# Optimization experiments

Hardware: AMD Instinct MI355X
Metric: run time of the kernel (lower is better)

The kernel has to match this reference:

```python
import jax, jax.numpy as jnp
import numpy as np

B, S, D, H = 2, 2048, 1024, 16
HD = D // H
EPS = 1e-5


def setup_inputs() -> dict:
    key = jax.random.key(0)
    ks = jax.random.split(key, 12)
    s = 1.0 / np.sqrt(D)
    inp = {
        "q": jax.random.normal(ks[0], (B, S, D), jnp.float32),
        "k": jax.random.normal(ks[1], (B, S, D), jnp.float32),
        "v": jax.random.normal(ks[2], (B, S, D), jnp.float32),
        "mask": jnp.ones((B, S, S), jnp.int32),
        "Wq": jax.random.normal(ks[3], (D, D), jnp.float32) * s,
        "bq": jnp.zeros((D,), jnp.float32),
        "Wk": jax.random.normal(ks[4], (D, D), jnp.float32) * s,
        "bk": jnp.zeros((D,), jnp.float32),
        "Wv": jax.random.normal(ks[5], (D, D), jnp.float32) * s,
        "bv": jnp.zeros((D,), jnp.float32),
        "Wo": jax.random.normal(ks[6], (D, D), jnp.float32) * s,
        "bo": jnp.zeros((D,), jnp.float32),
        "gamma": jnp.ones((D,), jnp.float32),
        "beta": jnp.zeros((D,), jnp.float32),
    }
    return inp


def reference(q, k, v, mask, Wq, bq, Wk, bk, Wv, bv, Wo, bo, gamma, beta):
    residual = q
    # projections (torch Linear: x @ W.T + b)
    qh = (q @ Wq.T + bq).reshape(B, S, H, HD).transpose(0, 2, 1, 3)  # b h s d
    kh = (k @ Wk.T + bk).reshape(B, S, H, HD).transpose(0, 2, 1, 3)
    vh = (v @ Wv.T + bv).reshape(B, S, H, HD).transpose(0, 2, 1, 3)
    scores = jnp.einsum('bhid,bhjd->bhij', qh, kh) / jnp.sqrt(jnp.float32(HD))
    scores = jnp.where(mask[:, None, :, :] == 0, jnp.float32(-1e9), scores)
    attention = jax.nn.softmax(scores, axis=-1)  # dropout=0 (eval)
    context = jnp.einsum('bhij,bhjd->bhid', attention, vh)
    context = context.transpose(0, 2, 1, 3).reshape(B, S, D)
    out = context @ Wo.T + bo
    x = out + residual
    mu = jnp.mean(x, axis=-1, keepdims=True)
    var = jnp.mean(jnp.square(x - mu), axis=-1, keepdims=True)
    output = (x - mu) * jax.lax.rsqrt(var + EPS) * gamma + beta
    return (output, attention)
```

## Files before the change

kernel.cpp:

```cpp
#include <hip/hip_runtime.h>
#include <hip/hip_bf16.h>


typedef float f32x4 __attribute__((ext_vector_type(4)));
typedef short short8 __attribute__((ext_vector_type(8)));

#if __has_builtin(__builtin_amdgcn_exp2f)
#define EXP2(x) __builtin_amdgcn_exp2f(x)
#else
#define EXP2(x) exp2f(x)
#endif

#define QSCALE 0.18033688011112042f
#define MASKNEG -1.4426950408889634e9f

#define BAR_DRAIN16() asm volatile("s_waitcnt vmcnt(16) lgkmcnt(0)\ns_barrier" ::: "memory")
#define BAR_LGKM()    asm volatile("s_waitcnt lgkmcnt(0)\ns_barrier" ::: "memory")

__device__ __forceinline__ short f2bs(float f) {
  union { __hip_bfloat16 h; short s; } u;
  u.h = __float2bfloat16(f);
  return u.s;
}

__device__ __forceinline__ void async16(const void* g, void* l) {
  __builtin_amdgcn_global_load_lds(
      (const __attribute__((address_space(1))) unsigned int*)g,
      (__attribute__((address_space(3))) unsigned int*)l, 16, 0, 0);
}

__global__ __launch_bounds__(256) void cvt_mask_kernel(
    const float* __restrict__ q, const float* __restrict__ k, const float* __restrict__ v,
    const float* __restrict__ wq, const float* __restrict__ wk, const float* __restrict__ wv,
    const float* __restrict__ wo, short* __restrict__ dst,
    const int* __restrict__ mask, unsigned* __restrict__ bits, unsigned* __restrict__ flags) {
  if (blockIdx.x < 8192) {
    long base = (long)blockIdx.x * 2048;
    const float* src;
    if      (base <  4194304) src = q  + base;
    else if (base <  8388608) src = k  + (base - 4194304);
    else if (base < 12582912) src = v  + (base - 8388608);
    else if (base < 13631488) src = wq + (base - 12582912);
    else if (base < 14680064) src = wk + (base - 13631488);
    else if (base < 15728640) src = wv + (base - 14680064);
    else                      src = wo + (base - 15728640);
    int off = threadIdx.x * 8;
    float4 a = *(const float4*)(src + off);
    float4 b = *(const float4*)(src + off + 4);
    short8 o;
    o[0] = f2bs(a.x); o[1] = f2bs(a.y); o[2] = f2bs(a.z); o[3] = f2bs(a.w);
    o[4] = f2bs(b.x); o[5] = f2bs(b.y); o[6] = f2bs(b.z); o[7] = f2bs(b.w);
    *(short8*)(dst + base + off) = o;
  } else {
    int bid = blockIdx.x - 8192;
    int t = threadIdx.x, w = t >> 6, lane = t & 63;
    for (int it = 0; it < 16; ++it) {
      long gw = (long)it * 8192 + bid * 4 + w;
      long base = gw * 64;
      int mv = mask[base + lane];
      unsigned long long m = __ballot(mv != 0);
      if (lane == 0)  bits[gw * 2]     = (unsigned)m;
      if (lane == 32) bits[gw * 2 + 1] = (unsigned)(m >> 32);
      if (lane == 0 && m != 0xFFFFFFFFFFFFFFFFull) {
        long j = base & 2047, i = (base >> 11) & 2047, b = base >> 22;
        atomicOr(&flags[(int)(b * 256 + (i >> 7) * 16 + (j >> 7))], 1u);
      }
    }
  }
}

__global__ __launch_bounds__(256, 2) void proj_kernel(
    const short* __restrict__ Abase, const short* __restrict__ Wbase,
    const float* __restrict__ bq, const float* __restrict__ bk, const float* __restrict__ bv,
    short* __restrict__ Qh, short* __restrict__ Kh, short* __restrict__ Vt) {
  __shared__ __align__(16) short As[2][128 * 64];
  __shared__ __align__(16) short Bs[2][128 * 64];
  const int mode = blockIdx.z;
  const short* A = Abase + (size_t)mode * 4194304;
  const short* W = Wbase + (size_t)mode * 1048576;
  const float* bias = (mode == 0) ? bq : (mode == 1 ? bk : bv);
  const int t = threadIdx.x, w = t >> 6, lane = t & 63, g = lane >> 4, lc = lane & 15;
  const int wrow = (w >> 1) * 64, wcol = (w & 1) * 64;
  const int m0 = blockIdx.x * 128, n0 = blockIdx.y * 128;

#define PSTAGE(buf, k0)                                                                     \
  do {                                                                                      \
    _Pragma("unroll") for (int i_ = 0; i_ < 4; i_++) {                                      \
      int cb = i_ * 256 + w * 64, ch = cb + lane, row = ch >> 3, c = ch & 7;                \
      int so = ((c ^ (row & 7)) << 3);                                                      \
      async16(A + (size_t)(m0 + row) * 1024 + (k0) + so, (void*)&As[buf][cb << 3]);         \
      async16(W + (size_t)(n0 + row) * 1024 + (k0) + so, (void*)&Bs[buf][cb << 3]);         \
    }                                                                                       \
  } while (0)

  f32x4 acc[4][4] = {};
  PSTAGE(0, 0);
  __syncthreads();
  int pb = 0;
  for (int kt = 0; kt < 16; ++kt) {
    if (kt < 15) PSTAGE(pb ^ 1, (kt + 1) * 64);
#pragma unroll
    for (int kf = 0; kf < 2; ++kf) {
      short8 af[4], bf[4];
#pragma unroll
      for (int m = 0; m < 4; m++) {
        int row = wrow + m * 16 + lc;
        af[m] = *(const short8*)&As[pb][(row << 6) + (((kf * 4 + g) ^ (row & 7)) << 3)];
      }
#pragma unroll
      for (int n = 0; n < 4; n++) {
        int row = wcol + n * 16 + lc;
        bf[n] = *(const short8*)&Bs[pb][(row << 6) + (((kf * 4 + g) ^ (row & 7)) << 3)];
      }
      __builtin_amdgcn_s_setprio(1);
#pragma unroll
      for (int m = 0; m < 4; m++)
#pragma unroll
        for (int n = 0; n < 4; n++)
          acc[m][n] = __builtin_amdgcn_mfma_f32_16x16x32_bf16(af[m], bf[n], acc[m][n], 0, 0, 0);
      __builtin_amdgcn_s_setprio(0);
    }
    __syncthreads();
    pb ^= 1;
  }
#undef PSTAGE
#pragma unroll
  for (int n = 0; n < 4; n++) {
    const int col = n0 + wcol + n * 16 + lc;
    const float bv_ = bias[col];
    const int h = col >> 6, d = col & 63;
#pragma unroll
    for (int m = 0; m < 4; m++)
#pragma unroll
      for (int r = 0; r < 4; r++) {
        const int srow = m0 + wrow + m * 16 + g * 4 + r;
        const int b = srow >> 11, s = srow & 2047;
        float val = acc[m][n][r] + bv_;
        if (mode == 0)
          Qh[((size_t)(b * 16 + h) * 2048 + s) * 64 + d] = f2bs(val * QSCALE);
        else if (mode == 1)
          Kh[((size_t)(b * 16 + h) * 2048 + s) * 64 + d] = f2bs(val);
        else
          Vt[((size_t)(b * 16 + h) * 64 + d) * 2048 + s] = f2bs(val);
      }
  }
}

__global__ __launch_bounds__(256, 2) void attn_kernel(
    const short* __restrict__ Qh, const short* __restrict__ Kh, const short* __restrict__ Vt,
    const unsigned* __restrict__ mbits, const unsigned* __restrict__ mflags,
    float* __restrict__ Pout, short* __restrict__ ctx) {
  __shared__ __align__(16) short Ks[2][128 * 64];
  __shared__ __align__(16) short Vs[64 * 128];
  __shared__ __align__(16) short Ps[128 * 128];
  const int L = blockIdx.x;
  const int xcd = L & 7, idx = L >> 3;
  const int bh = xcd + ((idx >> 4) << 3);
  const int qb = idx & 15;
  const int b = bh >> 4, h = bh & 15;
  const int t = threadIdx.x, w = t >> 6, lane = t & 63, g = lane >> 4, lc = lane & 15;
  const short* Qp = Qh + (size_t)bh * 2048 * 64;
  const short* Kp = Kh + (size_t)bh * 2048 * 64;
  const short* Vp = Vt + (size_t)bh * 64 * 2048;
  float* Pb = Pout + ((size_t)bh * 2048 + qb * 128) * 2048;

  short8 qf[2][2];
#pragma unroll
  for (int qm = 0; qm < 2; qm++)
#pragma unroll
    for (int kf = 0; kf < 2; kf++)
      qf[qm][kf] = *(const short8*)(Qp + (size_t)(qb * 128 + w * 32 + qm * 16 + lc) * 64 + kf * 32 + g * 8);

#define STAGE_K(buf, j0)                                                                   \
  do {                                                                                     \
    _Pragma("unroll") for (int i_ = 0; i_ < 4; i_++) {                                     \
      int cb = i_ * 256 + w * 64, ch = cb + lane, row = ch >> 3, c = ch & 7;               \
      int sc = c ^ (row & 7) ^ ((row >> 3) & 7);                                           \
      async16(Kp + (size_t)((j0) + row) * 64 + (sc << 3), (void*)&Ks[buf][cb << 3]);       \
    }                                                                                      \
  } while (0)
#define STAGE_V(j0)                                                                        \
  do {                                                                                     \
    _Pragma("unroll") for (int i_ = 0; i_ < 4; i_++) {                                     \
      int cb = i_ * 256 + w * 64, ch = cb + lane, row = ch >> 4, c = ch & 15;              \
      async16(Vp + (size_t)row * 2048 + (j0) + ((c ^ (row & 15)) << 3), (void*)&Vs[cb << 3]); \
    }                                                                                      \
  } while (0)

  float lsum[2] = {0.f, 0.f};
  int kb = 0;
  STAGE_K(0, 0);
  __syncthreads();
  for (int it = 0; it < 16; ++it) {
    if (it < 15) STAGE_K(kb ^ 1, (it + 1) * 128);
    f32x4 acc[2][8] = {};
    __builtin_amdgcn_s_setprio(1);
#pragma unroll
    for (int kf = 0; kf < 2; kf++)
#pragma unroll
      for (int n = 0; n < 8; n++) {
        int row = n * 16 + lc;
        int sc = (kf * 4 + g) ^ (row & 7) ^ ((row >> 3) & 7);
        short8 kfr = *(const short8*)&Ks[kb][(row << 6) + (sc << 3)];
        acc[0][n] = __builtin_amdgcn_mfma_f32_16x16x32_bf16(kfr, qf[0][kf], acc[0][n], 0, 0, 0);
        acc[1][n] = __builtin_amdgcn_mfma_f32_16x16x32_bf16(kfr, qf[1][kf], acc[1][n], 0, 0, 0);
      }
    __builtin_amdgcn_s_setprio(0);
    unsigned flg = mflags[b * 256 + qb * 16 + it];
    if (flg) {
#pragma unroll
      for (int qm = 0; qm < 2; qm++) {
        int ig = qb * 128 + w * 32 + qm * 16 + lc;
        uint4 mw = *(const uint4*)(mbits + ((size_t)b * 2048 + ig) * 64 + it * 4);
#pragma unroll
        for (int n = 0; n < 8; n++) {
          unsigned bw = (n >> 1) == 0 ? mw.x : ((n >> 1) == 1 ? mw.y : ((n >> 1) == 2 ? mw.z : mw.w));
#pragma unroll
          for (int r = 0; r < 4; r++)
            if (!((bw >> (((n & 1) << 4) + g * 4 + r)) & 1u)) acc[qm][n][r] = MASKNEG;
        }
      }
    }
#pragma unroll
    for (int qm = 0; qm < 2; qm++) {
      float s_ = 0.f;
#pragma unroll
      for (int n = 0; n < 8; n++)
#pragma unroll
        for (int r = 0; r < 4; r++) s_ += EXP2(acc[qm][n][r]);
      s_ += __shfl_xor(s_, 16);
      s_ += __shfl_xor(s_, 32);
      lsum[qm] += s_;
    }
    __syncthreads();
    kb ^= 1;
  }
  float* ls = (float*)Vs;
  if (g == 0) { ls[w * 32 + lc] = lsum[0]; ls[w * 32 + 16 + lc] = lsum[1]; }
  __syncthreads();
  float linv[8];
#pragma unroll
  for (int qm = 0; qm < 2; qm++)
#pragma unroll
    for (int r = 0; r < 4; r++) linv[qm * 4 + r] = 1.0f / ls[w * 32 + qm * 16 + g * 4 + r];
  kb = 0;
  STAGE_K(0, 0);
  __syncthreads();

  f32x4 acco[2][4] = {};
  for (int it = 0; it < 16; ++it) {
    const int j0 = it * 128;
    STAGE_V(j0);
    if (it < 15) STAGE_K(kb ^ 1, j0 + 128);
    f32x4 accs[2][8] = {};
    __builtin_amdgcn_s_setprio(1);
#pragma unroll
    for (int kf = 0; kf < 2; kf++)
#pragma unroll
      for (int n = 0; n < 8; n++) {
        int row = lc * 8 + n;
        int sc = (kf * 4 + g) ^ n ^ (lc & 7);
        short8 kfr = *(const short8*)&Ks[kb][(row << 6) + (sc << 3)];
        accs[0][n] = __builtin_amdgcn_mfma_f32_16x16x32_bf16(qf[0][kf], kfr, accs[0][n], 0, 0, 0);
        accs[1][n] = __builtin_amdgcn_mfma_f32_16x16x32_bf16(qf[1][kf], kfr, accs[1][n], 0, 0, 0);
      }
    __builtin_amdgcn_s_setprio(0);
    unsigned flg = mflags[b * 256 + qb * 16 + it];
    if (flg) {
#pragma unroll
      for (int qm = 0; qm < 2; qm++)
#pragma unroll
        for (int r = 0; r < 4; r++) {
          int ig = qb * 128 + w * 32 + qm * 16 + g * 4 + r;
          uint4 mw = *(const uint4*)(mbits + ((size_t)b * 2048 + ig) * 64 + it * 4);
          unsigned w01 = (lc & 4) ? mw.y : mw.x;
          unsigned w23 = (lc & 4) ? mw.w : mw.z;
          unsigned wsel = (lc & 8) ? w23 : w01;
#pragma unroll
          for (int n = 0; n < 8; n++)
            if (!((wsel >> (((lc & 3) << 3) + n)) & 1u)) accs[qm][n][r] = MASKNEG;
        }
    }
#pragma unroll
    for (int qm = 0; qm < 2; qm++)
#pragma unroll
      for (int r = 0; r < 4; r++) {
        const float li = linv[qm * 4 + r];
        const int irow = w * 32 + qm * 16 + g * 4 + r;
        f32x4 p0, p1;
#pragma unroll
        for (int n = 0; n < 4; n++) p0[n] = EXP2(accs[qm][n][r]) * li;
#pragma unroll
        for (int n = 0; n < 4; n++) p1[n] = EXP2(accs[qm][n + 4][r]) * li;
        float* pr = Pb + (size_t)irow * 2048 + j0 + (lc << 3);
        *(f32x4*)pr = p0;
        *(f32x4*)(pr + 4) = p1;
        short8 pk;
#pragma unroll
        for (int n = 0; n < 4; n++) { pk[n] = f2bs(p0[n]); pk[n + 4] = f2bs(p1[n]); }
        *(short8*)&Ps[(irow << 7) + ((lc ^ (irow & 15)) << 3)] = pk;
      }
    BAR_DRAIN16();
    __builtin_amdgcn_s_setprio(1);
#pragma unroll
    for (int kt4 = 0; kt4 < 4; kt4++) {
      short8 pa[2];
#pragma unroll
      for (int qm = 0; qm < 2; qm++) {
        int row = w * 32 + qm * 16 + lc;
        pa[qm] = *(const short8*)&Ps[(row << 7) + ((((kt4 << 2) + g) ^ (row & 15)) << 3)];
      }
#pragma unroll
      for (int dn = 0; dn < 4; dn++) {
        int d = dn * 16 + lc;
        short8 vb_ = *(const short8*)&Vs[(d << 7) + ((((kt4 << 2) + g) ^ (d & 15)) << 3)];
        acco[0][dn] = __builtin_amdgcn_mfma_f32_16x16x32_bf16(pa[0], vb_, acco[0][dn], 0, 0, 0);
        acco[1][dn] = __builtin_amdgcn_mfma_f32_16x16x32_bf16(pa[1], vb_, acco[1][dn], 0, 0, 0);
      }
    }
    __builtin_amdgcn_s_setprio(0);
    BAR_LGKM();
    kb ^= 1;
  }
#pragma unroll
  for (int qm = 0; qm < 2; qm++)
#pragma unroll
    for (int dn = 0; dn < 4; dn++)
#pragma unroll
      for (int r = 0; r < 4; r++) {
        int srow = qb * 128 + w * 32 + qm * 16 + g * 4 + r;
        int col = h * 64 + dn * 16 + lc;
        ctx[(size_t)(b * 2048 + srow) * 1024 + col] = f2bs(acco[qm][dn][r]);
      }
#undef STAGE_K
#undef STAGE_V
}

__global__ __launch_bounds__(256, 2) void oproj_kernel(
    const short* __restrict__ A, const short* __restrict__ W,
    const float* __restrict__ bo, const float* __restrict__ qres, float* __restrict__ xo) {
  __shared__ __align__(16) short As[2][128 * 64];
  __shared__ __align__(16) short Bs[2][128 * 64];
  const int t = threadIdx.x, w = t >> 6, lane = t & 63, g = lane >> 4, lc = lane & 15;
  const int wrow = (w >> 1) * 64, wcol = (w & 1) * 64;
  const int m0 = blockIdx.x * 128, n0 = blockIdx.y * 128;

#define OSTAGE(buf, k0)                                                                     \
  do {                                                                                      \
    _Pragma("unroll") for (int i_ = 0; i_ < 4; i_++) {                                      \
      int cb = i_ * 256 + w * 64, ch = cb + lane, row = ch >> 3, c = ch & 7;                \
      int so = ((c ^ (row & 7)) << 3);                                                      \
      async16(A + (size_t)(m0 + row) * 1024 + (k0) + so, (void*)&As[buf][cb << 3]);         \
      async16(W + (size_t)(n0 + row) * 1024 + (k0) + so, (void*)&Bs[buf][cb << 3]);         \
    }                                                                                       \
  } while (0)

  f32x4 acc[4][4] = {};
  OSTAGE(0, 0);
  __syncthreads();
  int pb = 0;
  for (int kt = 0; kt < 16; ++kt) {
    if (kt < 15) OSTAGE(pb ^ 1, (kt + 1) * 64);
#pragma unroll
    for (int kf = 0; kf < 2; ++kf) {
      short8 af[4], bf[4];
#pragma unroll
      for (int m = 0; m < 4; m++) {
        int row = wrow + m * 16 + lc;
        af[m] = *(const short8*)&As[pb][(row << 6) + (((kf * 4 + g) ^ (row & 7)) << 3)];
      }
#pragma unroll
      for (int n = 0; n < 4; n++) {
        int row = wcol + n * 16 + lc;
        bf[n] = *(const short8*)&Bs[pb][(row << 6) + (((kf * 4 + g) ^ (row & 7)) << 3)];
      }
      __builtin_amdgcn_s_setprio(1);
#pragma unroll
      for (int m = 0; m < 4; m++)
#pragma unroll
        for (int n = 0; n < 4; n++)
          acc[m][n] = __builtin_amdgcn_mfma_f32_16x16x32_bf16(af[m], bf[n], acc[m][n], 0, 0, 0);
      __builtin_amdgcn_s_setprio(0);
    }
    __syncthreads();
    pb ^= 1;
  }
#undef OSTAGE
#pragma unroll
  for (int n = 0; n < 4; n++) {
    const int col = n0 + wcol + n * 16 + lc;
    const float bv_ = bo[col];
#pragma unroll
    for (int m = 0; m < 4; m++)
#pragma unroll
      for (int r = 0; r < 4; r++) {
        const int srow = m0 + wrow + m * 16 + g * 4 + r;
        size_t o = (size_t)srow * 1024 + col;
        xo[o] = acc[m][n][r] + bv_ + qres[o];
      }
  }
}

__global__ __launch_bounds__(256) void ln_kernel(const float* __restrict__ x,
                                                 const float* __restrict__ gamma,
                                                 const float* __restrict__ beta,
                                                 float* __restrict__ out) {
  const int row = blockIdx.x, t = threadIdx.x;
  const float4 v = ((const float4*)(x + (size_t)row * 1024))[t];
  float s = v.x + v.y + v.z + v.w;
  float sq = v.x * v.x + v.y * v.y + v.z * v.z + v.w * v.w;
#pragma unroll
  for (int off = 1; off < 64; off <<= 1) { s += __shfl_xor(s, off); sq += __shfl_xor(sq, off); }
  __shared__ float ss[4], sqs[4];
  const int w = t >> 6, lane = t & 63;
  if (lane == 0) { ss[w] = s; sqs[w] = sq; }
  __syncthreads();
  s = ss[0] + ss[1] + ss[2] + ss[3];
  sq = sqs[0] + sqs[1] + sqs[2] + sqs[3];
  const float mu = s * (1.f / 1024.f);
  const float var = sq * (1.f / 1024.f) - mu * mu;
  const float rs = rsqrtf(var + 1e-5f);
  const float4 gm = ((const float4*)gamma)[t];
  const float4 bt = ((const float4*)beta)[t];
  float4 o;
  o.x = (v.x - mu) * rs * gm.x + bt.x;
  o.y = (v.y - mu) * rs * gm.y + bt.y;
  o.z = (v.z - mu) * rs * gm.z + bt.z;
  o.w = (v.w - mu) * rs * gm.w + bt.w;
  ((float4*)(out + (size_t)row * 1024))[t] = o;
}

extern "C" void kernel_launch(void* const* d_in, const int* in_sizes, int n_in,
                              void* d_out, int out_size, void* d_ws, size_t ws_size,
                              hipStream_t stream) {
  (void)in_sizes; (void)n_in; (void)out_size; (void)ws_size;
  const float* q     = (const float*)d_in[0];
  const float* k     = (const float*)d_in[1];
  const float* v     = (const float*)d_in[2];
  const int*   mask  = (const int*)d_in[3];
  const float* Wq    = (const float*)d_in[4];
  const float* bq    = (const float*)d_in[5];
  const float* Wk    = (const float*)d_in[6];
  const float* bk    = (const float*)d_in[7];
  const float* Wv    = (const float*)d_in[8];
  const float* bv    = (const float*)d_in[9];
  const float* Wo    = (const float*)d_in[10];
  const float* bo    = (const float*)d_in[11];
  const float* gamma = (const float*)d_in[12];
  const float* beta  = (const float*)d_in[13];

  char* ws = (char*)d_ws;
  short* cvtdst = (short*)ws;
  short* Qh     = (short*)(ws + 33554432);
  short* Kh     = (short*)(ws + 41943040);
  short* Vt     = (short*)(ws + 50331648);
  unsigned* mbits  = (unsigned*)(ws + 58720256);
  unsigned* mflags = (unsigned*)(ws + 59768832);
  float* x   = (float*)ws;
  short* ctx = (short*)(ws + 16777216);

  float* outln = (float*)d_out;
  float* Pout  = (float*)d_out + 4194304;

  hipMemsetAsync(mflags, 0, 2048, stream);
  cvt_mask_kernel<<<10240, 256, 0, stream>>>(q, k, v, Wq, Wk, Wv, Wo, cvtdst, mask, mbits, mflags);
  proj_kernel<<<dim3(32, 8, 3), 256, 0, stream>>>(cvtdst, cvtdst + 12582912, bq, bk, bv, Qh, Kh, Vt);
  attn_kernel<<<512, 256, 0, stream>>>(Qh, Kh, Vt, mbits, mflags, Pout, ctx);
  oproj_kernel<<<dim3(32, 8), 256, 0, stream>>>(ctx, cvtdst + 15728640, bo, q, x);
  ln_kernel<<<4096, 256, 0, stream>>>(x, gamma, beta, outln);
}
```

Before: 283.5 us.

## Move mask bit-packing into projection kernel and remap GEMM tiles per XCD

Mask bit-packing moves out of the conversion kernel and into the projection GEMM launch as extra trailing blocks, so the mask scan can overlap with the projection matmuls instead of the conversion pass. Both the projection and output-projection GEMMs switch to a 1D grid whose block index is remapped so that blocks landing on the same XCD share row tiles of A, aiming for better L2 reuse. In exchange, the mask blocks now compete for CUs with the GEMM blocks, and the remap assumes round-robin dispatch of blocks across eight XCDs.

```diff
diff --git a/kernel.cpp b/kernel.cpp
--- a/kernel.cpp
+++ b/kernel.cpp
@@ -29,30 +29,36 @@
       (__attribute__((address_space(3))) unsigned int*)l, 16, 0, 0);
 }
 
-__global__ __launch_bounds__(256) void cvt_mask_kernel(
+__global__ __launch_bounds__(256) void cvt_kernel(
     const float* __restrict__ q, const float* __restrict__ k, const float* __restrict__ v,
     const float* __restrict__ wq, const float* __restrict__ wk, const float* __restrict__ wv,
-    const float* __restrict__ wo, short* __restrict__ dst,
+    const float* __restrict__ wo, short* __restrict__ dst) {
+  long base = (long)blockIdx.x * 2048;
+  const float* src;
+  if      (base <  4194304) src = q  + base;
+  else if (base <  8388608) src = k  + (base - 4194304);
+  else if (base < 12582912) src = v  + (base - 8388608);
+  else if (base < 13631488) src = wq + (base - 12582912);
+  else if (base < 14680064) src = wk + (base - 13631488);
+  else if (base < 15728640) src = wv + (base - 14680064);
+  else                      src = wo + (base - 15728640);
+  int off = threadIdx.x * 8;
+  float4 a = *(const float4*)(src + off);
+  float4 b = *(const float4*)(src + off + 4);
+  short8 o;
+  o[0] = f2bs(a.x); o[1] = f2bs(a.y); o[2] = f2bs(a.z); o[3] = f2bs(a.w);
+  o[4] = f2bs(b.x); o[5] = f2bs(b.y); o[6] = f2bs(b.z); o[7] = f2bs(b.w);
+  *(short8*)(dst + base + off) = o;
+}
+
+__global__ __launch_bounds__(256, 2) void proj_mask_kernel(
+    const short* __restrict__ Abase, const short* __restrict__ Wbase,
+    const float* __restrict__ bq, const float* __restrict__ bk, const float* __restrict__ bv,
+    short* __restrict__ Qh, short* __restrict__ Kh, short* __restrict__ Vt,
     const int* __restrict__ mask, unsigned* __restrict__ bits, unsigned* __restrict__ flags) {
-  if (blockIdx.x < 8192) {
-    long base = (long)blockIdx.x * 2048;
-    const float* src;
-    if      (base <  4194304) src = q  + base;
-    else if (base <  8388608) src = k  + (base - 4194304);
-    else if (base < 12582912) src = v  + (base - 8388608);
-    else if (base < 13631488) src = wq + (base - 12582912);
-    else if (base < 14680064) src = wk + (base - 13631488);
-    else if (base < 15728640) src = wv + (base - 14680064);
-    else                      src = wo + (base - 15728640);
-    int off = threadIdx.x * 8;
-    float4 a = *(const float4*)(src + off);
-    float4 b = *(const float4*)(src + off + 4);
-    short8 o;
-    o[0] = f2bs(a.x); o[1] = f2bs(a.y); o[2] = f2bs(a.z); o[3] = f2bs(a.w);
-    o[4] = f2bs(b.x); o[5] = f2bs(b.y); o[6] = f2bs(b.z); o[7] = f2bs(b.w);
-    *(short8*)(dst + base + off) = o;
-  } else {
-    int bid = blockIdx.x - 8192;
+  const int id = blockIdx.x;
+  if (id >= 768) {
+    int bid = id - 768;
     int t = threadIdx.x, w = t >> 6, lane = t & 63;
     for (int it = 0; it < 16; ++it) {
       long gw = (long)it * 8192 + bid * 4 + w;
@@ -66,22 +72,20 @@
         atomicOr(&flags[(int)(b * 256 + (i >> 7) * 16 + (j >> 7))], 1u);
       }
     }
-  }
-}
-
-__global__ __launch_bounds__(256, 2) void proj_kernel(
-    const short* __restrict__ Abase, const short* __restrict__ Wbase,
-    const float* __restrict__ bq, const float* __restrict__ bk, const float* __restrict__ bv,
-    short* __restrict__ Qh, short* __restrict__ Kh, short* __restrict__ Vt) {
+    return;
+  }
+  const int xcd = id & 7, li = id >> 3;
+  const int mode = li >> 5;
+  const int r_ = li & 31;
+  const int m0 = (xcd * 4 + (r_ >> 3)) * 128;
+  const int n0 = (r_ & 7) * 128;
   __shared__ __align__(16) short As[2][128 * 64];
   __shared__ __align__(16) short Bs[2][128 * 64];
-  const int mode = blockIdx.z;
   const short* A = Abase + (size_t)mode * 4194304;
   const short* W = Wbase + (size_t)mode * 1048576;
   const float* bias = (mode == 0) ? bq : (mode == 1 ? bk : bv);
   const int t = threadIdx.x, w = t >> 6, lane = t & 63, g = lane >> 4, lc = lane & 15;
   const int wrow = (w >> 1) * 64, wcol = (w & 1) * 64;
-  const int m0 = blockIdx.x * 128, n0 = blockIdx.y * 128;
 
 #define PSTAGE(buf, k0)                                                                     \
   do {                                                                                      \
@@ -341,9 +345,12 @@
     const float* __restrict__ bo, const float* __restrict__ qres, float* __restrict__ xo) {
   __shared__ __align__(16) short As[2][128 * 64];
   __shared__ __align__(16) short Bs[2][128 * 64];
+  const int id = blockIdx.x;
+  const int xcd = id & 7, li = id >> 3;
+  const int m0 = (xcd * 4 + (li >> 3)) * 128;
+  const int n0 = (li & 7) * 128;
   const int t = threadIdx.x, w = t >> 6, lane = t & 63, g = lane >> 4, lc = lane & 15;
   const int wrow = (w >> 1) * 64, wcol = (w & 1) * 64;
-  const int m0 = blockIdx.x * 128, n0 = blockIdx.y * 128;
 
 #define OSTAGE(buf, k0)                                                                     \
   do {                                                                                      \
@@ -463,9 +470,10 @@
   float* Pout  = (float*)d_out + 4194304;
 
   hipMemsetAsync(mflags, 0, 2048, stream);
-  cvt_mask_kernel<<<10240, 256, 0, stream>>>(q, k, v, Wq, Wk, Wv, Wo, cvtdst, mask, mbits, mflags);
-  proj_kernel<<<dim3(32, 8, 3), 256, 0, stream>>>(cvtdst, cvtdst + 12582912, bq, bk, bv, Qh, Kh, Vt);
+  cvt_kernel<<<8192, 256, 0, stream>>>(q, k, v, Wq, Wk, Wv, Wo, cvtdst);
+  proj_mask_kernel<<<2816, 256, 0, stream>>>(cvtdst, cvtdst + 12582912, bq, bk, bv, Qh, Kh, Vt,
+                                             mask, mbits, mflags);
   attn_kernel<<<512, 256, 0, stream>>>(Qh, Kh, Vt, mbits, mflags, Pout, ctx);
-  oproj_kernel<<<dim3(32, 8), 256, 0, stream>>>(ctx, cvtdst + 15728640, bo, q, x);
+  oproj_kernel<<<256, 256, 0, stream>>>(ctx, cvtdst + 15728640, bo, q, x);
   ln_kernel<<<4096, 256, 0, stream>>>(x, gamma, beta, outln);
 }
```

New measurement: 307.7 us. +8.5%, slower.

## Split attention into row-sum pass kernel and output pass kernel

Applied to the files above, without the earlier changes.

Moves the first softmax pass (QK^T, masking, exp-sum) into its own kernel, which uses only the K shared-memory buffer and is launched with a higher occupancy bound, and writes the inverse row sums to a workspace buffer. The second kernel reads those inverse sums and does the normalized probability write and PV product. The aim is to run the compute-bound first pass at higher occupancy than the LDS-heavy second pass allows. In exchange it adds a kernel launch, a small global round-trip, and reloads Q in both kernels.

```diff
diff --git a/kernel.cpp b/kernel.cpp
--- a/kernel.cpp
+++ b/kernel.cpp
@@ -146,10 +146,96 @@
   }
 }
 
-__global__ __launch_bounds__(256, 2) void attn_kernel(
+__global__ __launch_bounds__(256, 4) void attnA_kernel(
+    const short* __restrict__ Qh, const short* __restrict__ Kh,
+    const unsigned* __restrict__ mbits, const unsigned* __restrict__ mflags,
+    float* __restrict__ lbuf) {
+  __shared__ __align__(16) short Ks[2][128 * 64];
+  const int L = blockIdx.x;
+  const int xcd = L & 7, idx = L >> 3;
+  const int bh = xcd + ((idx >> 4) << 3);
+  const int qb = idx & 15;
+  const int b = bh >> 4;
+  const int t = threadIdx.x, w = t >> 6, lane = t & 63, g = lane >> 4, lc = lane & 15;
+  const short* Qp = Qh + (size_t)bh * 2048 * 64;
+  const short* Kp = Kh + (size_t)bh * 2048 * 64;
+
+  short8 qf[2][2];
+#pragma unroll
+  for (int qm = 0; qm < 2; qm++)
+#pragma unroll
+    for (int kf = 0; kf < 2; kf++)
+      qf[qm][kf] = *(const short8*)(Qp + (size_t)(qb * 128 + w * 32 + qm * 16 + lc) * 64 + kf * 32 + g * 8);
+
+#define STAGE_KA(buf, j0)                                                                  \
+  do {                                                                                     \
+    _Pragma("unroll") for (int i_ = 0; i_ < 4; i_++) {                                     \
+      int cb = i_ * 256 + w * 64, ch = cb + lane, row = ch >> 3, c = ch & 7;               \
+      int sc = c ^ (row & 7) ^ ((row >> 3) & 7);                                           \
+      async16(Kp + (size_t)((j0) + row) * 64 + (sc << 3), (void*)&Ks[buf][cb << 3]);       \
+    }                                                                                      \
+  } while (0)
+
+  float lsum[2] = {0.f, 0.f};
+  int kb = 0;
+  STAGE_KA(0, 0);
+  __syncthreads();
+  for (int it = 0; it < 16; ++it) {
+    if (it < 15) STAGE_KA(kb ^ 1, (it + 1) * 128);
+    f32x4 acc[2][8] = {};
+    __builtin_amdgcn_s_setprio(1);
+#pragma unroll
+    for (int kf = 0; kf < 2; kf++)
+#pragma unroll
+      for (int n = 0; n < 8; n++) {
+        int row = n * 16 + lc;
+        int sc = (kf * 4 + g) ^ (row & 7) ^ ((row >> 3) & 7);
+        short8 kfr = *(const short8*)&Ks[kb][(row << 6) + (sc << 3)];
+        acc[0][n] = __builtin_amdgcn_mfma_f32_16x16x32_bf16(kfr, qf[0][kf], acc[0][n], 0, 0, 0);
+        acc[1][n] = __builtin_amdgcn_mfma_f32_16x16x32_bf16(kfr, qf[1][kf], acc[1][n], 0, 0, 0);
+      }
+    __builtin_amdgcn_s_setprio(0);
+    unsigned flg = mflags[b * 256 + qb * 16 + it];
+    if (flg) {
+#pragma unroll
+      for (int qm = 0; qm < 2; qm++) {
+        int ig = qb * 128 + w * 32 + qm * 16 + lc;
+        uint4 mw = *(const uint4*)(mbits + ((size_t)b * 2048 + ig) * 64 + it * 4);
+#pragma unroll
+        for (int n = 0; n < 8; n++) {
+          unsigned bw = (n >> 1) == 0 ? mw.x : ((n >> 1) == 1 ? mw.y : ((n >> 1) == 2 ? mw.z : mw.w));
+#pragma unroll
+          for (int r = 0; r < 4; r++)
+            if (!((bw >> (((n & 1) << 4) + g * 4 + r)) & 1u)) acc[qm][n][r] = MASKNEG;
+        }
+      }
+    }
+#pragma unroll
+    for (int qm = 0; qm < 2; qm++) {
+      float s_ = 0.f;
+#pragma unroll
+      for (int n = 0; n < 8; n++)
+#pragma unroll
+        for (int r = 0; r < 4; r++) s_ += EXP2(acc[qm][n][r]);
+      s_ += __shfl_xor(s_, 16);
+      s_ += __shfl_xor(s_, 32);
+      lsum[qm] += s_;
+    }
+    __syncthreads();
+    kb ^= 1;
+  }
+#undef STAGE_KA
+  if (g == 0) {
+    float* lb = lbuf + (size_t)(bh * 16 + qb) * 128;
+    lb[w * 32 + lc]      = 1.0f / lsum[0];
+    lb[w * 32 + 16 + lc] = 1.0f / lsum[1];
+  }
+}
+
+__global__ __launch_bounds__(256, 2) void attnB_kernel(
     const short* __restrict__ Qh, const short* __restrict__ Kh, const short* __restrict__ Vt,
     const unsigned* __restrict__ mbits, const unsigned* __restrict__ mflags,
-    float* __restrict__ Pout, short* __restrict__ ctx) {
+    const float* __restrict__ lbuf, float* __restrict__ Pout, short* __restrict__ ctx) {
   __shared__ __align__(16) short Ks[2][128 * 64];
   __shared__ __align__(16) short Vs[64 * 128];
   __shared__ __align__(16) short Ps[128 * 128];
@@ -170,6 +256,15 @@
 #pragma unroll
     for (int kf = 0; kf < 2; kf++)
       qf[qm][kf] = *(const short8*)(Qp + (size_t)(qb * 128 + w * 32 + qm * 16 + lc) * 64 + kf * 32 + g * 8);
+
+  float linv[8];
+  {
+    const float* lb = lbuf + (size_t)(bh * 16 + qb) * 128;
+#pragma unroll
+    for (int qm = 0; qm < 2; qm++)
+#pragma unroll
+      for (int r = 0; r < 4; r++) linv[qm * 4 + r] = lb[w * 32 + qm * 16 + g * 4 + r];
+  }
 
 #define STAGE_K(buf, j0)                                                                   \
   do {                                                                                     \
@@ -187,63 +282,7 @@
     }                                                                                      \
   } while (0)
 
-  float lsum[2] = {0.f, 0.f};
   int kb = 0;
-  STAGE_K(0, 0);
-  __syncthreads();
-  for (int it = 0; it < 16; ++it) {
-    if (it < 15) STAGE_K(kb ^ 1, (it + 1) * 128);
-    f32x4 acc[2][8] = {};
-    __builtin_amdgcn_s_setprio(1);
-#pragma unroll
-    for (int kf = 0; kf < 2; kf++)
-#pragma unroll
-      for (int n = 0; n < 8; n++) {
-        int row = n * 16 + lc;
-        int sc = (kf * 4 + g) ^ (row & 7) ^ ((row >> 3) & 7);
-        short8 kfr = *(const short8*)&Ks[kb][(row << 6) + (sc << 3)];
-        acc[0][n] = __builtin_amdgcn_mfma_f32_16x16x32_bf16(kfr, qf[0][kf], acc[0][n], 0, 0, 0);
-        acc[1][n] = __builtin_amdgcn_mfma_f32_16x16x32_bf16(kfr, qf[1][kf], acc[1][n], 0, 0, 0);
-      }
-    __builtin_amdgcn_s_setprio(0);
-    unsigned flg = mflags[b * 256 + qb * 16 + it];
-    if (flg) {
-#pragma unroll
-      for (int qm = 0; qm < 2; qm++) {
-        int ig = qb * 128 + w * 32 + qm * 16 + lc;
-        uint4 mw = *(const uint4*)(mbits + ((size_t)b * 2048 + ig) * 64 + it * 4);
-#pragma unroll
-        for (int n = 0; n < 8; n++) {
-          unsigned bw = (n >> 1) == 0 ? mw.x : ((n >> 1) == 1 ? mw.y : ((n >> 1) == 2 ? mw.z : mw.w));
-#pragma unroll
-          for (int r = 0; r < 4; r++)
-            if (!((bw >> (((n & 1) << 4) + g * 4 + r)) & 1u)) acc[qm][n][r] = MASKNEG;
-        }
-      }
-    }
-#pragma unroll
-    for (int qm = 0; qm < 2; qm++) {
-      float s_ = 0.f;
-#pragma unroll
-      for (int n = 0; n < 8; n++)
-#pragma unroll
-        for (int r = 0; r < 4; r++) s_ += EXP2(acc[qm][n][r]);
-      s_ += __shfl_xor(s_, 16);
-      s_ += __shfl_xor(s_, 32);
-      lsum[qm] += s_;
-    }
-    __syncthreads();
-    kb ^= 1;
-  }
-  float* ls = (float*)Vs;
-  if (g == 0) { ls[w * 32 + lc] = lsum[0]; ls[w * 32 + 16 + lc] = lsum[1]; }
-  __syncthreads();
-  float linv[8];
-#pragma unroll
-  for (int qm = 0; qm < 2; qm++)
-#pragma unroll
-    for (int r = 0; r < 4; r++) linv[qm * 4 + r] = 1.0f / ls[w * 32 + qm * 16 + g * 4 + r];
-  kb = 0;
   STAGE_K(0, 0);
   __syncthreads();
 
@@ -456,6 +495,7 @@
   short* Vt     = (short*)(ws + 50331648);
   unsigned* mbits  = (unsigned*)(ws + 58720256);
   unsigned* mflags = (unsigned*)(ws + 59768832);
+  float* lbuf  = (float*)(ws + 59771904);
   float* x   = (float*)ws;
   short* ctx = (short*)(ws + 16777216);
 
@@ -465,7 +505,8 @@
   hipMemsetAsync(mflags, 0, 2048, stream);
   cvt_mask_kernel<<<10240, 256, 0, stream>>>(q, k, v, Wq, Wk, Wv, Wo, cvtdst, mask, mbits, mflags);
   proj_kernel<<<dim3(32, 8, 3), 256, 0, stream>>>(cvtdst, cvtdst + 12582912, bq, bk, bv, Qh, Kh, Vt);
-  attn_kernel<<<512, 256, 0, stream>>>(Qh, Kh, Vt, mbits, mflags, Pout, ctx);
+  attnA_kernel<<<512, 256, 0, stream>>>(Qh, Kh, mbits, mflags, lbuf);
+  attnB_kernel<<<512, 256, 0, stream>>>(Qh, Kh, Vt, mbits, mflags, lbuf, Pout, ctx);
   oproj_kernel<<<dim3(32, 8), 256, 0, stream>>>(ctx, cvtdst + 15728640, bo, q, x);
   ln_kernel<<<4096, 256, 0, stream>>>(x, gamma, beta, outln);
 }
```

After: 334.3 us. +17.9%, slower.

## Split attention work across eight waves with sixteen query rows each

Applied to the files above, without the earlier changes.

The attention kernel moves from 256 to 512 threads per block. Each wave now owns 16 query rows instead of 32, so per-thread accumulators, Q fragments and the async staging loads are halved, and the barrier waits on 8 outstanding loads instead of 16. The aim is more waves per CU, which should hide the latency of the large probability-matrix stores and the exp work. In exchange, each K/V fragment read from LDS feeds only one MFMA instead of two, which doubles LDS read traffic per FLOP, and barriers now synchronise more waves.

```diff
diff --git a/kernel.cpp b/kernel.cpp
--- a/kernel.cpp
+++ b/kernel.cpp
@@ -14,7 +14,7 @@
 #define QSCALE 0.18033688011112042f
 #define MASKNEG -1.4426950408889634e9f
 
-#define BAR_DRAIN16() asm volatile("s_waitcnt vmcnt(16) lgkmcnt(0)\ns_barrier" ::: "memory")
+#define BAR_DRAIN8()  asm volatile("s_waitcnt vmcnt(8) lgkmcnt(0)\ns_barrier" ::: "memory")
 #define BAR_LGKM()    asm volatile("s_waitcnt lgkmcnt(0)\ns_barrier" ::: "memory")
 
 __device__ __forceinline__ short f2bs(float f) {
@@ -146,7 +146,7 @@
   }
 }
 
-__global__ __launch_bounds__(256, 2) void attn_kernel(
+__global__ __launch_bounds__(512, 4) void attn_kernel(
     const short* __restrict__ Qh, const short* __restrict__ Kh, const short* __restrict__ Vt,
     const unsigned* __restrict__ mbits, const unsigned* __restrict__ mflags,
     float* __restrict__ Pout, short* __restrict__ ctx) {
@@ -164,36 +164,34 @@
   const short* Vp = Vt + (size_t)bh * 64 * 2048;
   float* Pb = Pout + ((size_t)bh * 2048 + qb * 128) * 2048;
 
-  short8 qf[2][2];
-#pragma unroll
-  for (int qm = 0; qm < 2; qm++)
-#pragma unroll
-    for (int kf = 0; kf < 2; kf++)
-      qf[qm][kf] = *(const short8*)(Qp + (size_t)(qb * 128 + w * 32 + qm * 16 + lc) * 64 + kf * 32 + g * 8);
+  short8 qf[2];
+#pragma unroll
+  for (int kf = 0; kf < 2; kf++)
+    qf[kf] = *(const short8*)(Qp + (size_t)(qb * 128 + w * 16 + lc) * 64 + kf * 32 + g * 8);
 
 #define STAGE_K(buf, j0)                                                                   \
   do {                                                                                     \
-    _Pragma("unroll") for (int i_ = 0; i_ < 4; i_++) {                                     \
-      int cb = i_ * 256 + w * 64, ch = cb + lane, row = ch >> 3, c = ch & 7;               \
+    _Pragma("unroll") for (int i_ = 0; i_ < 2; i_++) {                                     \
+      int cb = i_ * 512 + w * 64, ch = cb + lane, row = ch >> 3, c = ch & 7;               \
       int sc = c ^ (row & 7) ^ ((row >> 3) & 7);                                           \
       async16(Kp + (size_t)((j0) + row) * 64 + (sc << 3), (void*)&Ks[buf][cb << 3]);       \
     }                                                                                      \
   } while (0)
 #define STAGE_V(j0)                                                                        \
   do {                                                                                     \
-    _Pragma("unroll") for (int i_ = 0; i_ < 4; i_++) {                                     \
-      int cb = i_ * 256 + w * 64, ch = cb + lane, row = ch >> 4, c = ch & 15;              \
+    _Pragma("unroll") for (int i_ = 0; i_ < 2; i_++) {                                     \
+      int cb = i_ * 512 + w * 64, ch = cb + lane, row = ch >> 4, c = ch & 15;              \
       async16(Vp + (size_t)row * 2048 + (j0) + ((c ^ (row & 15)) << 3), (void*)&Vs[cb << 3]); \
     }                                                                                      \
   } while (0)
 
-  float lsum[2] = {0.f, 0.f};
+  float lsum = 0.f;
   int kb = 0;
   STAGE_K(0, 0);
   __syncthreads();
   for (int it = 0; it < 16; ++it) {
     if (it < 15) STAGE_K(kb ^ 1, (it + 1) * 128);
-    f32x4 acc[2][8] = {};
+    f32x4 acc[8] = {};
     __builtin_amdgcn_s_setprio(1);
 #pragma unroll
     for (int kf = 0; kf < 2; kf++)
@@ -202,57 +200,48 @@
         int row = n * 16 + lc;
         int sc = (kf * 4 + g) ^ (row & 7) ^ ((row >> 3) & 7);
         short8 kfr = *(const short8*)&Ks[kb][(row << 6) + (sc << 3)];
-        acc[0][n] = __builtin_amdgcn_mfma_f32_16x16x32_bf16(kfr, qf[0][kf], acc[0][n], 0, 0, 0);
-        acc[1][n] = __builtin_amdgcn_mfma_f32_16x16x32_bf16(kfr, qf[1][kf], acc[1][n], 0, 0, 0);
+        acc[n] = __builtin_amdgcn_mfma_f32_16x16x32_bf16(kfr, qf[kf], acc[n], 0, 0, 0);
       }
     __builtin_amdgcn_s_setprio(0);
     unsigned flg = mflags[b * 256 + qb * 16 + it];
     if (flg) {
-#pragma unroll
-      for (int qm = 0; qm < 2; qm++) {
-        int ig = qb * 128 + w * 32 + qm * 16 + lc;
-        uint4 mw = *(const uint4*)(mbits + ((size_t)b * 2048 + ig) * 64 + it * 4);
-#pragma unroll
-        for (int n = 0; n < 8; n++) {
-          unsigned bw = (n >> 1) == 0 ? mw.x : ((n >> 1) == 1 ? mw.y : ((n >> 1) == 2 ? mw.z : mw.w));
-#pragma unroll
-          for (int r = 0; r < 4; r++)
-            if (!((bw >> (((n & 1) << 4) + g * 4 + r)) & 1u)) acc[qm][n][r] = MASKNEG;
-        }
-      }
-    }
-#pragma unroll
-    for (int qm = 0; qm < 2; qm++) {
-      float s_ = 0.f;
-#pragma unroll
-      for (int n = 0; n < 8; n++)
-#pragma unroll
-        for (int r = 0; r < 4; r++) s_ += EXP2(acc[qm][n][r]);
-      s_ += __shfl_xor(s_, 16);
-      s_ += __shfl_xor(s_, 32);
-      lsum[qm] += s_;
-    }
+      int ig = qb * 128 + w * 16 + lc;
+      uint4 mw = *(const uint4*)(mbits + ((size_t)b * 2048 + ig) * 64 + it * 4);
+#pragma unroll
+      for (int n = 0; n < 8; n++) {
+        unsigned bw = (n >> 1) == 0 ? mw.x : ((n >> 1) == 1 ? mw.y : ((n >> 1) == 2 ? mw.z : mw.w));
+#pragma unroll
+        for (int r = 0; r < 4; r++)
+          if (!((bw >> (((n & 1) << 4) + g * 4 + r)) & 1u)) acc[n][r] = MASKNEG;
+      }
+    }
+    float s_ = 0.f;
+#pragma unroll
+    for (int n = 0; n < 8; n++)
+#pragma unroll
+      for (int r = 0; r < 4; r++) s_ += EXP2(acc[n][r]);
+    s_ += __shfl_xor(s_, 16);
+    s_ += __shfl_xor(s_, 32);
+    lsum += s_;
     __syncthreads();
     kb ^= 1;
   }
   float* ls = (float*)Vs;
-  if (g == 0) { ls[w * 32 + lc] = lsum[0]; ls[w * 32 + 16 + lc] = lsum[1]; }
-  __syncthreads();
-  float linv[8];
-#pragma unroll
-  for (int qm = 0; qm < 2; qm++)
-#pragma unroll
-    for (int r = 0; r < 4; r++) linv[qm * 4 + r] = 1.0f / ls[w * 32 + qm * 16 + g * 4 + r];
+  if (g == 0) ls[w * 16 + lc] = lsum;
+  __syncthreads();
+  float linv[4];
+#pragma unroll
+  for (int r = 0; r < 4; r++) linv[r] = 1.0f / ls[w * 16 + g * 4 + r];
   kb = 0;
   STAGE_K(0, 0);
   __syncthreads();
 
-  f32x4 acco[2][4] = {};
+  f32x4 acco[4] = {};
   for (int it = 0; it < 16; ++it) {
     const int j0 = it * 128;
     STAGE_V(j0);
     if (it < 15) STAGE_K(kb ^ 1, j0 + 128);
-    f32x4 accs[2][8] = {};
+    f32x4 accs[8] = {};
     __builtin_amdgcn_s_setprio(1);
 #pragma unroll
     for (int kf = 0; kf < 2; kf++)
@@ -261,61 +250,51 @@
         int row = lc * 8 + n;
         int sc = (kf * 4 + g) ^ n ^ (lc & 7);
         short8 kfr = *(const short8*)&Ks[kb][(row << 6) + (sc << 3)];
-        accs[0][n] = __builtin_amdgcn_mfma_f32_16x16x32_bf16(qf[0][kf], kfr, accs[0][n], 0, 0, 0);
-        accs[1][n] = __builtin_amdgcn_mfma_f32_16x16x32_bf16(qf[1][kf], kfr, accs[1][n], 0, 0, 0);
+        accs[n] = __builtin_amdgcn_mfma_f32_16x16x32_bf16(qf[kf], kfr, accs[n], 0, 0, 0);
       }
     __builtin_amdgcn_s_setprio(0);
     unsigned flg = mflags[b * 256 + qb * 16 + it];
     if (flg) {
 #pragma unroll
-      for (int qm = 0; qm < 2; qm++)
-#pragma unroll
-        for (int r = 0; r < 4; r++) {
-          int ig = qb * 128 + w * 32 + qm * 16 + g * 4 + r;
-          uint4 mw = *(const uint4*)(mbits + ((size_t)b * 2048 + ig) * 64 + it * 4);
-          unsigned w01 = (lc & 4) ? mw.y : mw.x;
-          unsigned w23 = (lc & 4) ? mw.w : mw.z;
-          unsigned wsel = (lc & 8) ? w23 : w01;
-#pragma unroll
-          for (int n = 0; n < 8; n++)
-            if (!((wsel >> (((lc & 3) << 3) + n)) & 1u)) accs[qm][n][r] = MASKNEG;
-        }
-    }
-#pragma unroll
-    for (int qm = 0; qm < 2; qm++)
-#pragma unroll
       for (int r = 0; r < 4; r++) {
-        const float li = linv[qm * 4 + r];
-        const int irow = w * 32 + qm * 16 + g * 4 + r;
-        f32x4 p0, p1;
-#pragma unroll
-        for (int n = 0; n < 4; n++) p0[n] = EXP2(accs[qm][n][r]) * li;
-#pragma unroll
-        for (int n = 0; n < 4; n++) p1[n] = EXP2(accs[qm][n + 4][r]) * li;
-        float* pr = Pb + (size_t)irow * 2048 + j0 + (lc << 3);
-        *(f32x4*)pr = p0;
-        *(f32x4*)(pr + 4) = p1;
-        short8 pk;
-#pragma unroll
-        for (int n = 0; n < 4; n++) { pk[n] = f2bs(p0[n]); pk[n + 4] = f2bs(p1[n]); }
-        *(short8*)&Ps[(irow << 7) + ((lc ^ (irow & 15)) << 3)] = pk;
-      }
-    BAR_DRAIN16();
+        int ig = qb * 128 + w * 16 + g * 4 + r;
+        uint4 mw = *(const uint4*)(mbits + ((size_t)b * 2048 + ig) * 64 + it * 4);
+        unsigned w01 = (lc & 4) ? mw.y : mw.x;
+        unsigned w23 = (lc & 4) ? mw.w : mw.z;
+        unsigned wsel = (lc & 8) ? w23 : w01;
+#pragma unroll
+        for (int n = 0; n < 8; n++)
+          if (!((wsel >> (((lc & 3) << 3) + n)) & 1u)) accs[n][r] = MASKNEG;
+      }
+    }
+#pragma unroll
+    for (int r = 0; r < 4; r++) {
+      const float li = linv[r];
+      const int irow = w * 16 + g * 4 + r;
+      f32x4 p0, p1;
+#pragma unroll
+      for (int n = 0; n < 4; n++) p0[n] = EXP2(accs[n][r]) * li;
+#pragma unroll
+      for (int n = 0; n < 4; n++) p1[n] = EXP2(accs[n + 4][r]) * li;
+      float* pr = Pb + (size_t)irow * 2048 + j0 + (lc << 3);
+      *(f32x4*)pr = p0;
+      *(f32x4*)(pr + 4) = p1;
+      short8 pk;
+#pragma unroll
+      for (int n = 0; n < 4; n++) { pk[n] = f2bs(p0[n]); pk[n + 4] = f2bs(p1[n]); }
+      *(short8*)&Ps[(irow << 7) + ((lc ^ (irow & 15)) << 3)] = pk;
+    }
+    BAR_DRAIN8();
     __builtin_amdgcn_s_setprio(1);
 #pragma unroll
     for (int kt4 = 0; kt4 < 4; kt4++) {
-      short8 pa[2];
-#pragma unroll
-      for (int qm = 0; qm < 2; qm++) {
-        int row = w * 32 + qm * 16 + lc;
-        pa[qm] = *(const short8*)&Ps[(row << 7) + ((((kt4 << 2) + g) ^ (row & 15)) << 3)];
-      }
+      int prow = w * 16 + lc;
+      short8 pa = *(const short8*)&Ps[(prow << 7) + ((((kt4 << 2) + g) ^ (prow & 15)) << 3)];
 #pragma unroll
       for (int dn = 0; dn < 4; dn++) {
         int d = dn * 16 + lc;
         short8 vb_ = *(const short8*)&Vs[(d << 7) + ((((kt4 << 2) + g) ^ (d & 15)) << 3)];
-        acco[0][dn] = __builtin_amdgcn_mfma_f32_16x16x32_bf16(pa[0], vb_, acco[0][dn], 0, 0, 0);
-        acco[1][dn] = __builtin_amdgcn_mfma_f32_16x16x32_bf16(pa[1], vb_, acco[1][dn], 0, 0, 0);
+        acco[dn] = __builtin_amdgcn_mfma_f32_16x16x32_bf16(pa, vb_, acco[dn], 0, 0, 0);
       }
     }
     __builtin_amdgcn_s_setprio(0);
@@ -323,15 +302,13 @@
     kb ^= 1;
   }
 #pragma unroll
-  for (int qm = 0; qm < 2; qm++)
-#pragma unroll
-    for (int dn = 0; dn < 4; dn++)
-#pragma unroll
-      for (int r = 0; r < 4; r++) {
-        int srow = qb * 128 + w * 32 + qm * 16 + g * 4 + r;
-        int col = h * 64 + dn * 16 + lc;
-        ctx[(size_t)(b * 2048 + srow) * 1024 + col] = f2bs(acco[qm][dn][r]);
-      }
+  for (int dn = 0; dn < 4; dn++)
+#pragma unroll
+    for (int r = 0; r < 4; r++) {
+      int srow = qb * 128 + w * 16 + g * 4 + r;
+      int col = h * 64 + dn * 16 + lc;
+      ctx[(size_t)(b * 2048 + srow) * 1024 + col] = f2bs(acco[dn][r]);
+    }
 #undef STAGE_K
 #undef STAGE_V
 }
@@ -465,7 +442,7 @@
   hipMemsetAsync(mflags, 0, 2048, stream);
   cvt_mask_kernel<<<10240, 256, 0, stream>>>(q, k, v, Wq, Wk, Wv, Wo, cvtdst, mask, mbits, mflags);
   proj_kernel<<<dim3(32, 8, 3), 256, 0, stream>>>(cvtdst, cvtdst + 12582912, bq, bk, bv, Qh, Kh, Vt);
-  attn_kernel<<<512, 256, 0, stream>>>(Qh, Kh, Vt, mbits, mflags, Pout, ctx);
+  attn_kernel<<<512, 512, 0, stream>>>(Qh, Kh, Vt, mbits, mflags, Pout, ctx);
   oproj_kernel<<<dim3(32, 8), 256, 0, stream>>>(ctx, cvtdst + 15728640, bo, q, x);
   ln_kernel<<<4096, 256, 0, stream>>>(x, gamma, beta, outln);
 }
```

Measured after the change: 285.3 us. Within noise of the previous version (+0.6%).
